# Kernel tuning notes

Measured on AMD Instinct MI355X. Metric: run time of the kernel, lower is better.

The kernel has to match this reference:

```python
import jax, jax.numpy as jnp
import numpy as np

SCORE_THRESH = 0.05
NMS_THRESH = 0.5
DETS_PER_IMG = 100
IMG_W, IMG_H = 1333.0, 800.0
BBOX_XFORM_CLIP = float(np.log(1000.0 / 16.0))
WX, WY, WW, WH = 10.0, 10.0, 5.0, 5.0


def decode_boxes(rel, ref):
    widths = ref[:, 2] - ref[:, 0] + 1.0
    heights = ref[:, 3] - ref[:, 1] + 1.0
    ctr_x = ref[:, 0] + 0.5 * widths
    ctr_y = ref[:, 1] + 0.5 * heights
    dx = rel[:, 0] / WX
    dy = rel[:, 1] / WY
    dw = jnp.minimum(rel[:, 2] / WW, BBOX_XFORM_CLIP)
    dh = jnp.minimum(rel[:, 3] / WH, BBOX_XFORM_CLIP)
    pcx = dx * widths + ctr_x
    pcy = dy * heights + ctr_y
    pw = jnp.exp(dw) * widths
    ph = jnp.exp(dh) * heights
    return jnp.stack([pcx - 0.5 * pw, pcy - 0.5 * ph,
                      pcx + 0.5 * pw - 1.0, pcy + 0.5 * ph - 1.0], axis=1)


def pairwise_iou(b):
    # torchvision-style IoU (no +1), b: [n,4] xyxy
    area = (b[:, 2] - b[:, 0]) * (b[:, 3] - b[:, 1])
    lt = jnp.maximum(b[:, None, :2], b[None, :, :2])
    rb = jnp.minimum(b[:, None, 2:], b[None, :, 2:])
    wh = jnp.clip(rb - lt, 0.0)
    inter = wh[..., 0] * wh[..., 1]
    return inter / (area[:, None] + area[None, :] - inter + 1e-12)


def nms_keep(boxes, scores, valid):
    # masked greedy NMS; returns boolean keep mask in original order
    n = boxes.shape[0]
    order = jnp.argsort(-jnp.where(valid, scores, -jnp.inf))
    b = boxes[order]
    v = valid[order]
    iou = pairwise_iou(b)  # [n,n]
    idx = jnp.arange(n)

    def body(i, keep):
        suppressed = jnp.any(keep & (iou[i] > NMS_THRESH) & (idx < i))
        return keep.at[i].set(v[i] & ~suppressed)

    keep_sorted = jax.lax.fori_loop(0, n, body, jnp.zeros(n, dtype=bool))
    return jnp.zeros(n, dtype=bool).at[order].set(keep_sorted)


def setup_inputs() -> dict:
    key = jax.random.key(0)
    k1, k2, k3, k4, k5 = jax.random.split(key, 5)
    C, K = 16, 2048
    class_logit = jax.random.normal(k1, (C * K, 2), jnp.float32)
    box_regression = jax.random.normal(k2, (C * K, 8), jnp.float32) * 0.5
    x1 = jax.random.uniform(k3, (K,)) * (IMG_W - 220.0)
    y1 = jax.random.uniform(k4, (K,)) * (IMG_H - 220.0)
    wh = 20.0 + jax.random.uniform(k5, (K, 2)) * 180.0
    proposal_boxes = jnp.stack([x1, y1, x1 + wh[:, 0], y1 + wh[:, 1]], axis=1).astype(jnp.float32)
    unique_labels = jnp.arange(1, C + 1, dtype=jnp.int32)
    return {"class_logit": class_logit, "box_regression": box_regression,
            "proposal_boxes": proposal_boxes, "unique_labels": unique_labels}


def reference(class_logit, box_regression, proposal_boxes, unique_labels):
    C = unique_labels.shape[0]
    K = proposal_boxes.shape[0]
    # softmax over binary logits, take foreground prob
    prob = jax.nn.softmax(class_logit, axis=1)[:, 1]  # [C*K]
    rel = box_regression[:, 4:8]
    ref_boxes = jnp.tile(proposal_boxes, (C, 1))  # class-major [C*K,4]
    dec = decode_boxes(rel, ref_boxes)
    # clip_to_image (remove_empty=False), TO_REMOVE = 1
    dec = jnp.stack([jnp.clip(dec[:, 0], 0.0, IMG_W - 1.0),
                     jnp.clip(dec[:, 1], 0.0, IMG_H - 1.0),
                     jnp.clip(dec[:, 2], 0.0, IMG_W - 1.0),
                     jnp.clip(dec[:, 3], 0.0, IMG_H - 1.0)], axis=1)
    boxes_c = dec.reshape(C, K, 4)
    scores_c = prob.reshape(C, K)
    valid = scores_c > SCORE_THRESH
    keep = jax.vmap(nms_keep)(boxes_c, scores_c, valid).reshape(-1)  # [C*K]
    flat_scores = scores_c.reshape(-1)
    n_det = jnp.sum(keep)
    masked = jnp.where(keep, flat_scores, -jnp.inf)
    kth = jax.lax.top_k(masked, DETS_PER_IMG)[0][-1]  # 100th largest kept score
    keep_final = jnp.where(n_det > DETS_PER_IMG, keep & (flat_scores >= kth), keep)
    labels = jnp.broadcast_to(unique_labels[:, None], (C, K)).reshape(-1)
    out_boxes = jnp.where(keep_final[:, None], dec, 0.0)
    out_scores = jnp.where(keep_final, flat_scores, 0.0)
    out5 = jnp.concatenate([out_boxes, out_scores[:, None]], axis=1)  # [C*K,5]
    return out5, labels, keep_final
```

## Files before the change

### kernel.cpp

```cpp
#include <hip/hip_runtime.h>
#include <hip/hip_bf16.h>

#define NCLS 16
#define NBOX 2048
#define NTOT (NCLS * NBOX)
#define NCHUNK 32
#define SCORE_THRESH 0.05f
#define NMS_THRESH 0.5f
#define DETS_PER_IMG 100
#define TOPC 128
#define BBOX_CLIP 4.135166556742356f

typedef unsigned long long u64;

__device__ __forceinline__ u64 sel_mx(u64 a, u64 b, bool keepmax) {
    u64 mx = (a > b) ? a : b;
    u64 mn = (a > b) ? b : a;
    return keepmax ? mx : mn;
}

__global__ __launch_bounds__(1024) void sortmask_kernel(
    const float* __restrict__ logits,
    const float* __restrict__ regr,
    const float* __restrict__ props,
    float4* __restrict__ dec,
    u64* __restrict__ keys_out,
    u64* __restrict__ maskT,
    int* __restrict__ flags)
{
    int blk = blockIdx.x;
    int c = blk >> 4;
    int p = blk & 15;
    int tid = threadIdx.x;
    if (blk == 0 && tid == 0) { flags[0] = 0; flags[1] = 0; }

    int w = tid >> 6, l = tid & 63;
    int p0 = w * 128 + l;
    int p1 = p0 + 64;
    __shared__ u64 sk[NBOX];
    __shared__ float4 decv[NBOX];
    __shared__ float4 box[NBOX];

    u64 e01[2];
#pragma unroll
    for (int s = 0; s < 2; s++) {
#pragma clang fp contract(off)
        int t = s ? p1 : p0;
        int i = c * NBOX + t;
        float x0 = logits[2 * i + 0];
        float x1 = logits[2 * i + 1];
        float m = fmaxf(x0, x1);
        float e0f = expf(x0 - m);
        float e1f = expf(x1 - m);
        float score = e1f / (e0f + e1f);

        float px1 = props[4 * t + 0];
        float py1 = props[4 * t + 1];
        float px2 = props[4 * t + 2];
        float py2 = props[4 * t + 3];

        float bw = px2 - px1 + 1.0f;
        float bh = py2 - py1 + 1.0f;
        float cx = px1 + 0.5f * bw;
        float cy = py1 + 0.5f * bh;

        float dx = regr[8 * i + 4] / 10.0f;
        float dy = regr[8 * i + 5] / 10.0f;
        float dw = fminf(regr[8 * i + 6] / 5.0f, BBOX_CLIP);
        float dh = fminf(regr[8 * i + 7] / 5.0f, BBOX_CLIP);

        float pcx = dx * bw + cx;
        float pcy = dy * bh + cy;
        float pw  = expf(dw) * bw;
        float ph  = expf(dh) * bh;

        float b0 = pcx - 0.5f * pw;
        float b1 = pcy - 0.5f * ph;
        float b2 = pcx + 0.5f * pw - 1.0f;
        float b3 = pcy + 0.5f * ph - 1.0f;

        b0 = fminf(fmaxf(b0, 0.0f), 1332.0f);
        b1 = fminf(fmaxf(b1, 0.0f), 799.0f);
        b2 = fminf(fmaxf(b2, 0.0f), 1332.0f);
        b3 = fminf(fmaxf(b3, 0.0f), 799.0f);

        float4 bb = make_float4(b0, b1, b2, b3);
        decv[t] = bb;
        if (p == 0) dec[i] = bb;

        unsigned mono = 0u;
        if (score > SCORE_THRESH) mono = __float_as_uint(score) | 0x80000000u;
        e01[s] = ((u64)mono << 32) | (u64)(unsigned)(NBOX - 1 - t);
    }
    u64 e0 = e01[0], e1 = e01[1];

    for (int k = 2; k <= NBOX; k <<= 1) {
        bool desc0 = (p0 & k) == 0;
        bool desc1 = (p1 & k) == 0;
        for (int j = k >> 1; j > 0; j >>= 1) {
            if (j >= 128) {
                sk[p0] = e0; sk[p1] = e1;
                __syncthreads();
                u64 q0 = sk[p0 ^ j];
                u64 q1 = sk[p1 ^ j];
                e0 = sel_mx(e0, q0, desc0 ^ ((p0 & j) != 0));
                e1 = sel_mx(e1, q1, desc1 ^ ((p1 & j) != 0));
                __syncthreads();
            } else if (j == 64) {
                u64 mx = (e0 > e1) ? e0 : e1;
                u64 mn = (e0 > e1) ? e1 : e0;
                e0 = desc0 ? mx : mn;
                e1 = desc0 ? mn : mx;
            } else {
                u64 q0 = __shfl_xor(e0, j);
                u64 q1 = __shfl_xor(e1, j);
                bool hi = (l & j) != 0;
                e0 = sel_mx(e0, q0, desc0 ^ hi);
                e1 = sel_mx(e1, q1, desc1 ^ hi);
            }
        }
    }

    sk[p0] = e0; sk[p1] = e1;
    __syncthreads();

    for (int t = tid; t < NBOX; t += 1024) {
        u64 key = sk[t];
        if (p == 0) keys_out[c * NBOX + t] = key;
        int idx = (NBOX - 1) - (int)(key & 0xFFFFFFFFull);
        box[t] = decv[idx];
    }
    __syncthreads();

    int r = tid & 63;
    int g = tid >> 6;

    for (int pass = 0; pass < 2; pass++) {
#pragma clang fp contract(off)
        int Jc = pass ? (31 - p) : p;
        int j = Jc * 64 + r;
        float4 jb = box[j];
        float jar = (jb.z - jb.x) * (jb.w - jb.y);
        float hj = 0.5f * jar;
        float colC = hj + 5e-13f;

        for (int I = g; I <= Jc; I += 16) {
            u64 wm = 0;
            int rbase = I * 64;
#pragma unroll
            for (int i2 = 0; i2 < 64; i2++) {
#pragma clang fp contract(off)
                int gi = rbase + i2;
                float4 rb = box[gi];
                float ar = (rb.z - rb.x) * (rb.w - rb.y);
                float rha = 0.5f * ar;
                float lx = fmaxf(rb.x, jb.x);
                float ly = fmaxf(rb.y, jb.y);
                float rx = fminf(rb.z, jb.z);
                float ry = fminf(rb.w, jb.w);
                float ww = fmaxf(rx - lx, 0.0f);
                float hh = fmaxf(ry - ly, 0.0f);
                float inter = ww * hh;
                float s  = rha + colC;
                float band = 2e-6f * s;
                float delta = fmaf(1.5f, inter, -s);
                bool over = delta > band;
                bool amb = fabsf(delta) <= band;
                if (__any(amb)) {
                    float un = ar + jar - inter + 1e-12f;
                    float iou = inter / un;
                    bool ovx = iou > NMS_THRESH;
                    over = amb ? ovx : over;
                }
                if (over) wm |= 1ull << i2;
            }
            if (I == Jc) wm &= (1ull << r) - 1ull;
            maskT[((size_t)c * NCHUNK + I) * NBOX + j] = wm;
        }
    }
}

__global__ __launch_bounds__(64) void resolve_kernel(
    const u64* __restrict__ keys,
    const u64* __restrict__ maskT,
    const float4* __restrict__ dec,
    const int* __restrict__ ulabels,
    unsigned* __restrict__ compact,
    int* __restrict__ nkept,
    int* __restrict__ stats,
    int* __restrict__ flags,
    float* __restrict__ out)
{
    int c = blockIdx.x;
    int l = threadIdx.x;
    const u64* MT = maskT + (size_t)c * NCHUNK * NBOX;
    const u64* K  = keys + (size_t)c * NBOX;

    __shared__ unsigned keep_lds[NBOX];
    __shared__ unsigned ls[NCLS * TOPC];

    unsigned sup = 0;
    int offset = 0;
    u64 tm[2][NCHUNK - 1];

#pragma unroll
    for (int t = 0; t < NCHUNK - 1; t++)
        tm[0][t] = MT[(size_t)(1 + t) * 64 + l];
    u64 diag = MT[l];
    u64 key  = K[l];

#pragma unroll
    for (int I = 0; I < NCHUNK; I++) {
        u64 diagN = diag, keyN = key;
        if (I + 1 < NCHUNK) {
            const u64* rowpN = MT + (size_t)(I + 1) * NBOX + l;
#pragma unroll
            for (int t = 0; t < NCHUNK - 2 - I; t++)
                tm[(I + 1) & 1][t] = rowpN[(size_t)(I + 2 + t) * 64];
            diagN = MT[(size_t)(I + 1) * NBOX + (size_t)(I + 1) * 64 + l];
            keyN  = K[(I + 1) * 64 + l];
        }
        __builtin_amdgcn_sched_barrier(0);

        unsigned mono = (unsigned)(key >> 32);
        bool av = (mono != 0u) && (((sup >> I) & 1u) == 0u);
        u64 kept = 0;
        u64 availB = __ballot(av);
        while (availB) {
            u64 front = __ballot(av && ((diag & availB) == 0ull));
            kept |= front;
            bool fr = ((front >> l) & 1ull) != 0ull;
            bool sp = ((diag & front) != 0ull);
            av = av && !fr && !sp;
            availB = __ballot(av);
        }

        int idx = (NBOX - 1) - (int)(key & 0xFFFFFFFFull);
        bool isk = ((kept >> l) & 1ull) != 0ull;
        keep_lds[idx] = isk ? (mono & 0x7FFFFFFFu) : 0u;

        int pos = offset + __popcll(kept & ((1ull << l) - 1ull));
        if (isk && pos < TOPC) compact[c * TOPC + pos] = mono;
        offset += __popcll(kept);

#pragma unroll
        for (int t = 0; t < NCHUNK - 1 - I; t++)
            sup |= (tm[I & 1][t] & kept) ? (1u << (I + 1 + t)) : 0u;

        diag = diagN;
        key  = keyN;
    }

    for (int t = offset + l; t < TOPC; t += 64) compact[c * TOPC + t] = 0u;
    if (l == 0) nkept[c] = offset;
    __syncthreads();
    __threadfence();

    int got = 0;
    if (l == 0) got = atomicAdd(&flags[0], 1);
    got = __shfl(got, 0);

    if (got == NCLS - 1) {
        __threadfence();
        for (int t = l; t < NCLS * TOPC; t += 64) ls[t] = compact[t];
        int n_c = (l < NCLS) ? nkept[l] : 0;
        __syncthreads();

        int nd = n_c;
#pragma unroll
        for (int off = 32; off > 0; off >>= 1) nd += __shfl_down(nd, off);
        nd = __shfl(nd, 0);

        unsigned kth = 0u;
        if (nd > DETS_PER_IMG) {
            const unsigned* my = &ls[(l & 15) * TOPC];
            bool active = (l < NCLS);
            unsigned prefix = 0u;
            for (int bit = 31; bit >= 0; bit--) {
                unsigned cand = prefix | (1u << bit);
                int cnt = 0;
                if (active) {
                    if (my[TOPC - 1] >= cand) cnt = TOPC;
                    else {
                        int pos = 0;
#pragma unroll
                        for (int step = 64; step >= 1; step >>= 1)
                            if (my[pos + step - 1] >= cand) pos += step;
                        cnt = pos;
                    }
                }
#pragma unroll
                for (int off = 32; off > 0; off >>= 1) cnt += __shfl_down(cnt, off);
                cnt = __shfl(cnt, 0);
                if (cnt >= DETS_PER_IMG) prefix = cand;
            }
            kth = prefix & 0x7FFFFFFFu;
        }

        if (l == 0) {
            stats[0] = nd;
            stats[1] = (int)kth;
            __threadfence();
            __hip_atomic_store(&flags[1], 1, __ATOMIC_RELEASE,
                               __HIP_MEMORY_SCOPE_AGENT);
        }
        __syncthreads();
    } else {
        if (l == 0) {
            while (__hip_atomic_load(&flags[1], __ATOMIC_ACQUIRE,
                                     __HIP_MEMORY_SCOPE_AGENT) == 0) {}
        }
        __syncthreads();
    }

    int n_det = stats[0];
    unsigned kth = (unsigned)stats[1];
    float lab = (float)ulabels[c];
    for (int t = l; t < NBOX; t += 64) {
        unsigned kb = keep_lds[t];
        bool kf = kb && (n_det <= DETS_PER_IMG || kb >= kth);
        int i = c * NBOX + t;
        float4 b = dec[i];
        float* o5 = out + (size_t)i * 5;
        if (kf) {
            o5[0] = b.x; o5[1] = b.y; o5[2] = b.z; o5[3] = b.w;
            o5[4] = __uint_as_float(kb);
        } else {
            o5[0] = 0.0f; o5[1] = 0.0f; o5[2] = 0.0f; o5[3] = 0.0f; o5[4] = 0.0f;
        }
        out[NTOT * 5 + i] = lab;
        out[NTOT * 5 + NTOT + i] = kf ? 1.0f : 0.0f;
    }
}

extern "C" void kernel_launch(void* const* d_in, const int* in_sizes, int n_in,
                              void* d_out, int out_size, void* d_ws, size_t ws_size,
                              hipStream_t stream) {
    (void)in_sizes; (void)n_in; (void)out_size; (void)ws_size;

    const float* class_logit    = (const float*)d_in[0];
    const float* box_regression = (const float*)d_in[1];
    const float* proposal_boxes = (const float*)d_in[2];
    const int*   unique_labels  = (const int*)d_in[3];

    char* ws = (char*)d_ws;
    float4* dec        = (float4*)(ws + 0);
    u64* keys          = (u64*)(ws + 524288);
    u64* maskT         = (u64*)(ws + 786432);
    unsigned* compact  = (unsigned*)(ws + 9175040);
    int* nkept         = (int*)(ws + 9183232);
    int* stats         = (int*)(ws + 9183296);
    int* flags         = (int*)(ws + 9183360);

    float* out = (float*)d_out;

    sortmask_kernel<<<NCLS * 16, 1024, 0, stream>>>(class_logit, box_regression,
                                                    proposal_boxes, dec, keys,
                                                    maskT, flags);
    resolve_kernel<<<NCLS, 64, 0, stream>>>(keys, maskT, dec, unique_labels,
                                            compact, nkept, stats, flags, out);
}
```

Before: 149.9 us.

## Split final selection and output write into a separate wide kernel

Replaces the last-block-arrives atomic handshake and spin-wait in the resolve kernel with a third kernel launch. The new kernel recomputes the global kth threshold per block and writes outputs with 128 blocks of 256 threads instead of 16 single-wave blocks each looping over 2048 boxes. This widens the output-write phase and removes the cross-block spin, at the cost of an extra launch, a global keepbits round trip, and redundant kth computation in every block.

```diff
diff --git a/kernel.cpp b/kernel.cpp
--- a/kernel.cpp
+++ b/kernel.cpp
@@ -25,14 +25,12 @@
     const float* __restrict__ props,
     float4* __restrict__ dec,
     u64* __restrict__ keys_out,
-    u64* __restrict__ maskT,
-    int* __restrict__ flags)
+    u64* __restrict__ maskT)
 {
     int blk = blockIdx.x;
     int c = blk >> 4;
     int p = blk & 15;
     int tid = threadIdx.x;
-    if (blk == 0 && tid == 0) { flags[0] = 0; flags[1] = 0; }
 
     int w = tid >> 6, l = tid & 63;
     int p0 = w * 128 + l;
@@ -183,21 +181,14 @@
 __global__ __launch_bounds__(64) void resolve_kernel(
     const u64* __restrict__ keys,
     const u64* __restrict__ maskT,
-    const float4* __restrict__ dec,
-    const int* __restrict__ ulabels,
+    unsigned* __restrict__ keepbits,
     unsigned* __restrict__ compact,
-    int* __restrict__ nkept,
-    int* __restrict__ stats,
-    int* __restrict__ flags,
-    float* __restrict__ out)
+    int* __restrict__ nkept)
 {
     int c = blockIdx.x;
     int l = threadIdx.x;
     const u64* MT = maskT + (size_t)c * NCHUNK * NBOX;
     const u64* K  = keys + (size_t)c * NBOX;
-
-    __shared__ unsigned keep_lds[NBOX];
-    __shared__ unsigned ls[NCLS * TOPC];
 
     unsigned sup = 0;
     int offset = 0;
@@ -237,7 +228,7 @@
 
         int idx = (NBOX - 1) - (int)(key & 0xFFFFFFFFull);
         bool isk = ((kept >> l) & 1ull) != 0ull;
-        keep_lds[idx] = isk ? (mono & 0x7FFFFFFFu) : 0u;
+        keepbits[c * NBOX + idx] = isk ? (mono & 0x7FFFFFFFu) : 0u;
 
         int pos = offset + __popcll(kept & ((1ull << l) - 1ull));
         if (isk && pos < TOPC) compact[c * TOPC + pos] = mono;
@@ -253,19 +244,26 @@
 
     for (int t = offset + l; t < TOPC; t += 64) compact[c * TOPC + t] = 0u;
     if (l == 0) nkept[c] = offset;
+}
+
+__global__ __launch_bounds__(256) void selectwrite_kernel(
+    const unsigned* __restrict__ compact,
+    const int* __restrict__ nkept,
+    const unsigned* __restrict__ keepbits,
+    const float4* __restrict__ dec,
+    const int* __restrict__ ulabels,
+    float* __restrict__ out)
+{
+    __shared__ unsigned ls[NCLS * TOPC];
+    __shared__ int s_stats[2];
+    int tid = threadIdx.x;
+
+    for (int t = tid; t < NCLS * TOPC; t += 256) ls[t] = compact[t];
     __syncthreads();
-    __threadfence();
-
-    int got = 0;
-    if (l == 0) got = atomicAdd(&flags[0], 1);
-    got = __shfl(got, 0);
-
-    if (got == NCLS - 1) {
-        __threadfence();
-        for (int t = l; t < NCLS * TOPC; t += 64) ls[t] = compact[t];
+
+    if (tid < 64) {
+        int l = tid;
         int n_c = (l < NCLS) ? nkept[l] : 0;
-        __syncthreads();
-
         int nd = n_c;
 #pragma unroll
         for (int off = 32; off > 0; off >>= 1) nd += __shfl_down(nd, off);
@@ -296,41 +294,29 @@
             }
             kth = prefix & 0x7FFFFFFFu;
         }
-
-        if (l == 0) {
-            stats[0] = nd;
-            stats[1] = (int)kth;
-            __threadfence();
-            __hip_atomic_store(&flags[1], 1, __ATOMIC_RELEASE,
-                               __HIP_MEMORY_SCOPE_AGENT);
-        }
-        __syncthreads();
+        if (l == 0) { s_stats[0] = nd; s_stats[1] = (int)kth; }
+    }
+    __syncthreads();
+
+    int n_det = s_stats[0];
+    unsigned kth = (unsigned)s_stats[1];
+
+    int i = blockIdx.x * 256 + tid;
+    unsigned kb = keepbits[i];
+    bool kf = kb && (n_det <= DETS_PER_IMG || kb >= kth);
+
+    float4 b = dec[i];
+    float* o5 = out + (size_t)i * 5;
+    if (kf) {
+        o5[0] = b.x; o5[1] = b.y; o5[2] = b.z; o5[3] = b.w;
+        o5[4] = __uint_as_float(kb);
     } else {
-        if (l == 0) {
-            while (__hip_atomic_load(&flags[1], __ATOMIC_ACQUIRE,
-                                     __HIP_MEMORY_SCOPE_AGENT) == 0) {}
-        }
-        __syncthreads();
-    }
-
-    int n_det = stats[0];
-    unsigned kth = (unsigned)stats[1];
-    float lab = (float)ulabels[c];
-    for (int t = l; t < NBOX; t += 64) {
-        unsigned kb = keep_lds[t];
-        bool kf = kb && (n_det <= DETS_PER_IMG || kb >= kth);
-        int i = c * NBOX + t;
-        float4 b = dec[i];
-        float* o5 = out + (size_t)i * 5;
-        if (kf) {
-            o5[0] = b.x; o5[1] = b.y; o5[2] = b.z; o5[3] = b.w;
-            o5[4] = __uint_as_float(kb);
-        } else {
-            o5[0] = 0.0f; o5[1] = 0.0f; o5[2] = 0.0f; o5[3] = 0.0f; o5[4] = 0.0f;
-        }
-        out[NTOT * 5 + i] = lab;
-        out[NTOT * 5 + NTOT + i] = kf ? 1.0f : 0.0f;
-    }
+        o5[0] = 0.0f; o5[1] = 0.0f; o5[2] = 0.0f; o5[3] = 0.0f; o5[4] = 0.0f;
+    }
+
+    int c = i >> 11;
+    out[NTOT * 5 + i] = (float)ulabels[c];
+    out[NTOT * 5 + NTOT + i] = kf ? 1.0f : 0.0f;
 }
 
 extern "C" void kernel_launch(void* const* d_in, const int* in_sizes, int n_in,
@@ -347,16 +333,17 @@
     float4* dec        = (float4*)(ws + 0);
     u64* keys          = (u64*)(ws + 524288);
     u64* maskT         = (u64*)(ws + 786432);
-    unsigned* compact  = (unsigned*)(ws + 9175040);
-    int* nkept         = (int*)(ws + 9183232);
-    int* stats         = (int*)(ws + 9183296);
-    int* flags         = (int*)(ws + 9183360);
+    unsigned* keepbits = (unsigned*)(ws + 9175040);
+    unsigned* compact  = (unsigned*)(ws + 9306112);
+    int* nkept         = (int*)(ws + 9314304);
 
     float* out = (float*)d_out;
 
     sortmask_kernel<<<NCLS * 16, 1024, 0, stream>>>(class_logit, box_regression,
                                                     proposal_boxes, dec, keys,
-                                                    maskT, flags);
-    resolve_kernel<<<NCLS, 64, 0, stream>>>(keys, maskT, dec, unique_labels,
-                                            compact, nkept, stats, flags, out);
-}
+                                                    maskT);
+    resolve_kernel<<<NCLS, 64, 0, stream>>>(keys, maskT, keepbits,
+                                            compact, nkept);
+    selectwrite_kernel<<<NTOT / 256, 256, 0, stream>>>(compact, nkept, keepbits,
+                                                       dec, unique_labels, out);
+}
```

Result: faster. 137.8 us (-8.1%).
